# Performance work log

Measured on AMD Instinct MI355X. Metric: run time of the kernel, lower is better.

Reference implementation:

```python
import jax, jax.numpy as jnp
import numpy as np

WS = (8, 8)          # window_size -> S = 64
NUM_HEADS = 4
DIM = 128


def _relative_position_index(ws):
    wh, ww = ws
    coords = np.stack(np.meshgrid(np.arange(wh), np.arange(ww), indexing='ij'))  # (2,Wh,Ww)
    cf = coords.reshape(2, -1)                                   # (2, Wh*Ww)
    rel = cf[:, :, None] - cf[:, None, :]                        # (2, S, S)
    rel = rel.transpose(1, 2, 0).astype(np.int64)                # (S, S, 2)
    rel[:, :, 0] += wh - 1
    rel[:, :, 1] += ww - 1
    rel[:, :, 0] *= 2 * ww - 1
    return rel.sum(-1)                                           # (S, S)


def setup_inputs() -> dict:
    key = jax.random.key(0)
    k = jax.random.split(key, 6)
    B, S, N, C = 128, WS[0] * WS[1], 32, DIM
    num_rel = (2 * WS[0] - 1) * (2 * WS[1] - 1)
    return {
        'x': jax.random.normal(k[0], (B, S, N, C), dtype=jnp.float32),
        'qkv_w': jax.random.normal(k[1], (3 * C, C), dtype=jnp.float32) * 0.02,
        'qkv_b': jnp.zeros((3 * C,), dtype=jnp.float32),
        'proj_w': jax.random.normal(k[2], (C, C), dtype=jnp.float32) * 0.02,
        'proj_b': jnp.zeros((C,), dtype=jnp.float32),
        'bias_table': jax.random.normal(k[3], (num_rel, NUM_HEADS), dtype=jnp.float32) * 0.02,
    }


def reference(x, qkv_w, qkv_b, proj_w, proj_b, bias_table):
    B, S, N, C = x.shape
    H = NUM_HEADS
    D = N * C // H                      # effective head dim
    scale = (C // H) ** -0.5            # matches head_dim = dim // num_heads in __init__

    xf = x.reshape(B, S * N, C)
    qkv = xf @ qkv_w.T + qkv_b          # (B, S*N, 3C)
    qkv = qkv.reshape(B, S, 3, H, D).transpose(2, 0, 3, 1, 4)  # (3, B, H, S, D)
    q, k, v = qkv[0], qkv[1], qkv[2]

    rel_idx = jnp.asarray(_relative_position_index(WS))        # (S, S) int
    bias = bias_table[rel_idx.reshape(-1)].reshape(S, S, H).transpose(2, 0, 1)  # (H,S,S)

    attn = jnp.einsum('bhsd,bhtd->bhst', q, k) * scale + bias[None]
    attn = jax.nn.softmax(attn, axis=-1)

    out = jnp.einsum('bhst,bhtd->bhsd', attn, v)               # (B,H,S,D)
    out = out.transpose(0, 2, 1, 3).reshape(B, S * N, C)
    out = out @ proj_w.T + proj_b
    return out.reshape(B, S, N, C)
```

## Files before the change

### kernel.cpp

```cpp
#include <hip/hip_runtime.h>
#include <cmath>


typedef short bf16x8 __attribute__((ext_vector_type(8)));
typedef float f32x4  __attribute__((ext_vector_type(4)));
#define MFMA16 __builtin_amdgcn_mfma_f32_16x16x32_bf16

__device__ __forceinline__ unsigned rne16(float f) {
    unsigned u = __float_as_uint(f);
    return (u + 0x7fffu + ((u >> 16) & 1u)) & 0xffff0000u;
}
__device__ __forceinline__ void cvt8(float4 a, float4 b, bf16x8& H, bf16x8& L) {
    float f[8] = {a.x, a.y, a.z, a.w, b.x, b.y, b.z, b.w};
    #pragma unroll
    for (int i = 0; i < 8; ++i) {
        unsigned r = rne16(f[i]);
        H[i] = (short)(r >> 16);
        float fh = __uint_as_float(r);
        L[i] = (short)(rne16(f[i] - fh) >> 16);
    }
}
__device__ __forceinline__ void cvt8h(float4 a, float4 b, bf16x8& H) {
    float f[8] = {a.x, a.y, a.z, a.w, b.x, b.y, b.z, b.w};
    #pragma unroll
    for (int i = 0; i < 8; ++i) H[i] = (short)(rne16(f[i]) >> 16);
}

__global__ void split_w(const float* __restrict__ qw, unsigned short* __restrict__ wsp) {
    int idx = blockIdx.x * 256 + threadIdx.x;
    if (idx >= 49152) return;
    int j = idx >> 7, c = idx & 127;
    float v = qw[idx];
    unsigned r = rne16(v);
    unsigned rl = rne16(v - __uint_as_float(r));
    int dest = (((j >> 5) * 16 + (c >> 3)) * 32 + (j & 31)) * 8 + (c & 7);
    wsp[dest] = (unsigned short)(r >> 16);
    wsp[49152 + dest] = (unsigned short)(rl >> 16);
}
__global__ void split_pw(const float* __restrict__ pw, unsigned short* __restrict__ pwsp) {
    int idx = blockIdx.x * 256 + threadIdx.x;
    if (idx >= 16384) return;
    int cp = idx >> 7, c = idx & 127;
    float v = pw[idx];
    unsigned r = rne16(v);
    unsigned rl = rne16(v - __uint_as_float(r));
    int dest = ((c >> 3) * 128 + cp) * 8 + (c & 7);
    pwsp[dest] = (unsigned short)(r >> 16);
    pwsp[16384 + dest] = (unsigned short)(rl >> 16);
}

constexpr int A4_QC0 = 0,     A4_KC0 = 16640;
constexpr int A4_QC1 = 33280, A4_KC1 = 49920;
constexpr int A4_P   = 66560;
constexpr int A4_SMA = 74880;
constexpr int A4_SMB = 75392;
constexpr int A4_VC0 = 0,     A4_VC1 = 16640;
constexpr int A4_LDS = 75904;

__global__ __launch_bounds__(512, 4)
void attn_mfma4(const float* __restrict__ x,
                const float* __restrict__ qkv_b,
                const float* __restrict__ bias_table,
                const unsigned short* __restrict__ wsp,
                float* __restrict__ out)
{
    __shared__ __attribute__((aligned(128))) char lds[A4_LDS];
    const int tid = threadIdx.x;
    const int lane = tid & 63;
    const int w = tid >> 6;
    const int l15 = lane & 15, lg = lane >> 4;
    const int qt = w & 3, ch = w >> 2;
    const int rowbase = qt * 16;
    const int b = blockIdx.x >> 2, h = blockIdx.x & 3;
    const float* __restrict__ xb = x + (size_t)b * 262144;
    const float* xrow0 = xb + (size_t)(rowbase + l15) * 4096 + lg * 8;

    bf16x8 aH[4];
    bf16x8 kH[4];
    int cur_na = -1, cur_nk = -1;

    auto loadfrags = [&](int n0, bf16x8 (&H)[4]) {
        const float* p = xrow0 + (size_t)n0 * 128;
        #pragma unroll
        for (int ks = 0; ks < 4; ++ks) {
            float4 a = *(const float4*)(p + ks * 32);
            float4 c = *(const float4*)(p + ks * 32 + 4);
            cvt8h(a, c, H[ks]);
        }
    };

    auto prod64 = [&](const bf16x8 (&H)[4], int j0, f32x4 (&acc)[4]) {
        const unsigned short* wb = wsp + (size_t)(j0 >> 5) * 4096;
        #pragma unroll
        for (int ks = 0; ks < 4; ++ks) {
            #pragma unroll
            for (int ct = 0; ct < 4; ++ct) {
                int gct = ch * 4 + ct;
                int ro = (gct >> 1) * 4096 + ((ks * 4 + lg) * 32 + (gct & 1) * 16 + l15) * 8;
                bf16x8 bh = *(const bf16x8*)(wb + ro);
                acc[ct] = MFMA16(H[ks], bh, acc[ct], 0, 0, 0);
            }
        }
    };

    auto storeP64 = [&](int base, f32x4 (&acc)[4], int j0) {
        #pragma unroll
        for (int ct = 0; ct < 4; ++ct) {
            int d = (ch * 4 + ct) * 16 + l15;
            float bias = qkv_b[j0 + d];
            int dofs = (d >> 3) * 1040 + (d & 7) * 2;
            #pragma unroll
            for (int reg = 0; reg < 4; ++reg) {
                int s = rowbase + lg * 4 + reg;
                *(unsigned short*)(lds + base + dofs + s * 16) =
                    (unsigned short)(rne16(acc[ct][reg] + bias) >> 16);
            }
        }
    };

    f32x4 accQK[2];
    #pragma unroll
    for (int tt = 0; tt < 2; ++tt) accQK[tt] = (f32x4){0.f, 0.f, 0.f, 0.f};

    for (int cc = 0; cc < 8; ++cc) {
        int qcb = (cc & 1) ? A4_QC1 : A4_QC0;
        int kcb = (cc & 1) ? A4_KC1 : A4_KC0;
        int remq = h * 1024 + 128 * cc;
        int nq = remq / 384, j0q = remq - nq * 384;
        int remk = 4096 + h * 1024 + 128 * cc;
        int nk = remk / 384, j0k = remk - nk * 384;
        if (nq != cur_na) { loadfrags(nq, aH); cur_na = nq; }
        if (nk != cur_nk) { loadfrags(nk, kH); cur_nk = nk; }

        f32x4 qa[4];
        #pragma unroll
        for (int i = 0; i < 4; ++i) qa[i] = (f32x4){0.f, 0.f, 0.f, 0.f};
        prod64(aH, j0q, qa);
        storeP64(qcb, qa, j0q);

        f32x4 ka[4];
        #pragma unroll
        for (int i = 0; i < 4; ++i) ka[i] = (f32x4){0.f, 0.f, 0.f, 0.f};
        prod64(kH, j0k, ka);
        storeP64(kcb, ka, j0k);

        __syncthreads();

        #pragma unroll
        for (int kst = 0; kst < 4; ++kst) {
            int grp = (kst * 4 + lg) * 1040;
            bf16x8 qh = *(const bf16x8*)(lds + qcb + grp + (rowbase + l15) * 16);
            #pragma unroll
            for (int tt = 0; tt < 2; ++tt) {
                int trow = ((ch * 2 + tt) * 16 + l15) * 16;
                bf16x8 kh = *(const bf16x8*)(lds + kcb + grp + trow);
                accQK[tt] = MFMA16(qh, kh, accQK[tt], 0, 0, 0);
            }
        }
    }

    {
        const float scale = 0.17677669529663687f;
        float* smA = (float*)(lds + A4_SMA);
        float* smB = (float*)(lds + A4_SMB);
        float ex[4][2];
        #pragma unroll
        for (int reg = 0; reg < 4; ++reg) {
            int s = rowbase + lg * 4 + reg;
            int i1 = s >> 3, j1 = s & 7;
            float m = -1e30f;
            #pragma unroll
            for (int tt = 0; tt < 2; ++tt) {
                int t = (ch * 2 + tt) * 16 + l15;
                int i2 = t >> 3, j2 = t & 7;
                float L = accQK[tt][reg] * scale
                        + bias_table[((i1 - i2 + 7) * 15 + (j1 - j2 + 7)) * 4 + h];
                ex[reg][tt] = L;
                m = fmaxf(m, L);
            }
            m = fmaxf(m, __shfl_xor(m, 1));
            m = fmaxf(m, __shfl_xor(m, 2));
            m = fmaxf(m, __shfl_xor(m, 4));
            m = fmaxf(m, __shfl_xor(m, 8));
            if (l15 == 0) smA[ch * 64 + s] = m;
        }
        __syncthreads();
        #pragma unroll
        for (int reg = 0; reg < 4; ++reg) {
            int s = rowbase + lg * 4 + reg;
            float mg = fmaxf(smA[s], smA[64 + s]);
            float e0 = __expf(ex[reg][0] - mg);
            float e1 = __expf(ex[reg][1] - mg);
            ex[reg][0] = e0; ex[reg][1] = e1;
            float sum = e0 + e1;
            sum += __shfl_xor(sum, 1);
            sum += __shfl_xor(sum, 2);
            sum += __shfl_xor(sum, 4);
            sum += __shfl_xor(sum, 8);
            if (l15 == 0) smB[ch * 64 + s] = sum;
        }
        __syncthreads();
        #pragma unroll
        for (int reg = 0; reg < 4; ++reg) {
            int s = rowbase + lg * 4 + reg;
            float inv = 1.f / (smB[s] + smB[64 + s]);
            #pragma unroll
            for (int tt = 0; tt < 2; ++tt) {
                int t = (ch * 2 + tt) * 16 + l15;
                int off = (t >> 3) * 1040 + s * 16 + (t & 7) * 2;
                *(unsigned short*)(lds + A4_P + off) =
                    (unsigned short)(rne16(ex[reg][tt] * inv) >> 16);
            }
        }
    }

    cur_na = -1;
    float* ob = out + (size_t)b * 262144;
    for (int cc = 0; cc < 8; ++cc) {
        int vcb = (cc & 1) ? A4_VC1 : A4_VC0;
        int remv = 8192 + h * 1024 + 128 * cc;
        int nv = remv / 384, j0v = remv - nv * 384;
        if (nv != cur_na) { loadfrags(nv, aH); cur_na = nv; }

        f32x4 va[4];
        #pragma unroll
        for (int i = 0; i < 4; ++i) va[i] = (f32x4){0.f, 0.f, 0.f, 0.f};
        prod64(aH, j0v, va);

        #pragma unroll
        for (int ct = 0; ct < 4; ++ct) {
            int d = (ch * 4 + ct) * 16 + l15;
            float bias = qkv_b[j0v + d];
            #pragma unroll
            for (int reg = 0; reg < 4; ++reg) {
                int t = rowbase + lg * 4 + reg;
                int off = (t >> 3) * 2080 + d * 16 + (t & 7) * 2;
                *(unsigned short*)(lds + vcb + off) =
                    (unsigned short)(rne16(va[ct][reg] + bias) >> 16);
            }
        }
        __syncthreads();

        f32x4 o[4];
        #pragma unroll
        for (int i = 0; i < 4; ++i) o[i] = (f32x4){0.f, 0.f, 0.f, 0.f};
        #pragma unroll
        for (int kst = 0; kst < 2; ++kst) {
            bf16x8 pf = *(const bf16x8*)(lds + A4_P + (kst * 4 + lg) * 1040 + (rowbase + l15) * 16);
            int vgrp = (kst * 4 + lg) * 2080;
            #pragma unroll
            for (int dt = 0; dt < 4; ++dt) {
                int drow = ((ch * 4 + dt) * 16 + l15) * 16;
                bf16x8 vh = *(const bf16x8*)(lds + vcb + vgrp + drow);
                o[dt] = MFMA16(pf, vh, o[dt], 0, 0, 0);
            }
        }

        #pragma unroll
        for (int reg = 0; reg < 4; ++reg) {
            int s = rowbase + lg * 4 + reg;
            float* orow = ob + (size_t)(s * 32 + h * 8 + cc) * 128;
            #pragma unroll
            for (int dt = 0; dt < 4; ++dt)
                orow[(ch * 4 + dt) * 16 + l15] = o[dt][reg];
        }
    }
}

__global__ __launch_bounds__(256, 4)
void proj_mfma(const unsigned short* __restrict__ pwsp,
               const float* __restrict__ pb,
               float* __restrict__ io)
{
    const int tid = threadIdx.x;
    const int lane = tid & 63;
    const int w = tid >> 6;
    const int l15 = lane & 15, lg = lane >> 4;
    const size_t rbase = (size_t)blockIdx.x * 64 + w * 16;

    const float* rp = io + (rbase + l15) * 128 + lg * 8;
    bf16x8 aH[4], aL[4];
    #pragma unroll
    for (int ks = 0; ks < 4; ++ks) {
        float4 a = *(const float4*)(rp + ks * 32);
        float4 c = *(const float4*)(rp + ks * 32 + 4);
        cvt8(a, c, aH[ks], aL[ks]);
    }

    f32x4 acc[8];
    #pragma unroll
    for (int i = 0; i < 8; ++i) acc[i] = (f32x4){0.f, 0.f, 0.f, 0.f};

    #pragma unroll
    for (int ks = 0; ks < 4; ++ks) {
        #pragma unroll
        for (int ct = 0; ct < 8; ++ct) {
            int ro = ((ks * 4 + lg) * 128 + ct * 16 + l15) * 8;
            bf16x8 bh = *(const bf16x8*)(pwsp + ro);
            bf16x8 bl = *(const bf16x8*)(pwsp + 16384 + ro);
            acc[ct] = MFMA16(aH[ks], bh, acc[ct], 0, 0, 0);
            acc[ct] = MFMA16(aH[ks], bl, acc[ct], 0, 0, 0);
            acc[ct] = MFMA16(aL[ks], bh, acc[ct], 0, 0, 0);
        }
    }

    #pragma unroll
    for (int ct = 0; ct < 8; ++ct) {
        float bias = pb[ct * 16 + l15];
        #pragma unroll
        for (int reg = 0; reg < 4; ++reg)
            io[(rbase + lg * 4 + reg) * 128 + ct * 16 + l15] = acc[ct][reg] + bias;
    }
}

constexpr int QC_OFF = 0;
constexpr int KC_OFF = 8320;
constexpr int VC_OFF = 24960;
constexpr int P_OFF  = 41856;
constexpr int LDS_TOT = 50176;

__global__ __launch_bounds__(256, 2)
void attn_mfma(const float* __restrict__ x,
               const float* __restrict__ qkv_b,
               const float* __restrict__ bias_table,
               const unsigned short* __restrict__ wsp,
               float* __restrict__ out)
{
    __shared__ __attribute__((aligned(128))) char lds[LDS_TOT];
    const int tid = threadIdx.x;
    const int lane = tid & 63;
    const int w = tid >> 6;
    const int l15 = lane & 15, lg = lane >> 4;
    const int rowbase = 16 * w;
    const int b = blockIdx.x >> 2, h = blockIdx.x & 3;
    const float* __restrict__ xb = x + (size_t)b * 262144;
    const float* xrow0 = xb + ((size_t)(rowbase + l15) * 32) * 128 + lg * 8;

    bf16x8 aH[4], aL[4];
    bf16x8 kH[4], kL[4];
    int cur_na = -1, cur_nk = -1;

    auto loadfrags = [&](int n0, bf16x8 (&H)[4], bf16x8 (&L)[4]) {
        const float* p = xrow0 + (size_t)n0 * 128;
        #pragma unroll
        for (int ks = 0; ks < 4; ++ks) {
            float4 a = *(const float4*)(p + ks * 32);
            float4 c = *(const float4*)(p + ks * 32 + 4);
            cvt8(a, c, H[ks], L[ks]);
        }
    };

    auto mm_band = [&](const bf16x8 (&H)[4], const bf16x8 (&L)[4], int band,
                       f32x4& a0, f32x4& a1) {
        const unsigned short* wb = wsp + (size_t)band * 4096;
        #pragma unroll
        for (int ks = 0; ks < 4; ++ks) {
            int ro = ((ks * 4 + lg) * 32 + l15) * 8;
            bf16x8 b0h = *(const bf16x8*)(wb + ro);
            bf16x8 b0l = *(const bf16x8*)(wb + 49152 + ro);
            bf16x8 b1h = *(const bf16x8*)(wb + ro + 128);
            bf16x8 b1l = *(const bf16x8*)(wb + 49152 + ro + 128);
            a0 = MFMA16(H[ks], b0h, a0, 0, 0, 0);
            a0 = MFMA16(H[ks], b0l, a0, 0, 0, 0);
            a0 = MFMA16(L[ks], b0h, a0, 0, 0, 0);
            a1 = MFMA16(H[ks], b1h, a1, 0, 0, 0);
            a1 = MFMA16(H[ks], b1l, a1, 0, 0, 0);
            a1 = MFMA16(L[ks], b1h, a1, 0, 0, 0);
        }
    };

    auto store_rc = [&](char* base, f32x4 a0, f32x4 a1, float b0, float b1) {
        #pragma unroll
        for (int reg = 0; reg < 4; ++reg) {
            int s = rowbase + lg * 4 + reg;
            {
                float v = a0[reg] + b0;
                int i = l15;
                int off = (i >> 3) * 1040 + s * 16 + (i & 7) * 2;
                unsigned r = rne16(v);
                *(unsigned short*)(base + off) = (unsigned short)(r >> 16);
                *(unsigned short*)(base + 4160 + off) =
                    (unsigned short)(rne16(v - __uint_as_float(r)) >> 16);
            }
            {
                float v = a1[reg] + b1;
                int i = 16 + l15;
                int off = (i >> 3) * 1040 + s * 16 + (i & 7) * 2;
                unsigned r = rne16(v);
                *(unsigned short*)(base + off) = (unsigned short)(r >> 16);
                *(unsigned short*)(base + 4160 + off) =
                    (unsigned short)(rne16(v - __uint_as_float(r)) >> 16);
            }
        }
    };

    f32x4 accQK[4];
    #pragma unroll
    for (int tt = 0; tt < 4; ++tt) accQK[tt] = (f32x4){0.f, 0.f, 0.f, 0.f};

    int buf = 0;
    for (int ccc = 0; ccc < 32; ++ccc) {
        int remq = h * 1024 + 32 * ccc;
        int nq = remq / 384, j0q = remq - nq * 384, bandq = j0q >> 5;
        int remk = 4096 + h * 1024 + 32 * ccc;
        int nk = remk / 384, j0k = remk - nk * 384, bandk = j0k >> 5;
        if (nq != cur_na) { loadfrags(nq, aH, aL); cur_na = nq; }
        if (nk != cur_nk) { loadfrags(nk, kH, kL); cur_nk = nk; }

        f32x4 q0 = (f32x4){0.f,0.f,0.f,0.f}, q1 = (f32x4){0.f,0.f,0.f,0.f};
        mm_band(aH, aL, bandq, q0, q1);
        store_rc(lds + QC_OFF, q0, q1, qkv_b[j0q + l15], qkv_b[j0q + 16 + l15]);

        f32x4 k0 = (f32x4){0.f,0.f,0.f,0.f}, k1 = (f32x4){0.f,0.f,0.f,0.f};
        mm_band(kH, kL, bandk, k0, k1);
        store_rc(lds + KC_OFF + buf * 8320, k0, k1, qkv_b[j0k + l15], qkv_b[j0k + 16 + l15]);

        __syncthreads();

        const char* qc = lds + QC_OFF + lg * 1040 + (rowbase + l15) * 16;
        bf16x8 qah = *(const bf16x8*)qc;
        bf16x8 qal = *(const bf16x8*)(qc + 4160);
        #pragma unroll
        for (int tt = 0; tt < 4; ++tt) {
            const char* kc = lds + KC_OFF + buf * 8320 + lg * 1040 + (tt * 16 + l15) * 16;
            bf16x8 kbh = *(const bf16x8*)kc;
            bf16x8 kbl = *(const bf16x8*)(kc + 4160);
            accQK[tt] = MFMA16(qah, kbh, accQK[tt], 0, 0, 0);
            accQK[tt] = MFMA16(qah, kbl, accQK[tt], 0, 0, 0);
            accQK[tt] = MFMA16(qal, kbh, accQK[tt], 0, 0, 0);
        }
        buf ^= 1;
    }

    {
        const float scale = 0.17677669529663687f;
        #pragma unroll
        for (int reg = 0; reg < 4; ++reg) {
            int s = rowbase + lg * 4 + reg;
            int i1 = s >> 3, j1 = s & 7;
            float Lv[4];
            float m = -1e30f;
            #pragma unroll
            for (int tt = 0; tt < 4; ++tt) {
                int t = tt * 16 + l15;
                int i2 = t >> 3, j2 = t & 7;
                float L = accQK[tt][reg] * scale
                        + bias_table[((i1 - i2 + 7) * 15 + (j1 - j2 + 7)) * 4 + h];
                Lv[tt] = L;
                m = fmaxf(m, L);
            }
            m = fmaxf(m, __shfl_xor(m, 1));
            m = fmaxf(m, __shfl_xor(m, 2));
            m = fmaxf(m, __shfl_xor(m, 4));
            m = fmaxf(m, __shfl_xor(m, 8));
            float sum = 0.f;
            #pragma unroll
            for (int tt = 0; tt < 4; ++tt) { Lv[tt] = __expf(Lv[tt] - m); sum += Lv[tt]; }
            sum += __shfl_xor(sum, 1);
            sum += __shfl_xor(sum, 2);
            sum += __shfl_xor(sum, 4);
            sum += __shfl_xor(sum, 8);
            float inv = 1.f / sum;
            #pragma unroll
            for (int tt = 0; tt < 4; ++tt) {
                int t = tt * 16 + l15;
                int off = (t >> 3) * 1040 + s * 16 + (t & 7) * 2;
                *(unsigned short*)(lds + P_OFF + off) = (unsigned short)(rne16(Lv[tt] * inv) >> 16);
            }
        }
    }

    cur_na = -1;
    int bufv = 0;
    float* ob = out + (size_t)b * 262144;
    for (int ccc = 0; ccc < 32; ++ccc) {
        int remv = 8192 + h * 1024 + 32 * ccc;
        int nv = remv / 384, j0v = remv - nv * 384, bandv = j0v >> 5;
        if (nv != cur_na) { loadfrags(nv, aH, aL); cur_na = nv; }

        f32x4 v0 = (f32x4){0.f,0.f,0.f,0.f}, v1 = (f32x4){0.f,0.f,0.f,0.f};
        mm_band(aH, aL, bandv, v0, v1);
        {
            char* base = lds + VC_OFF + bufv * 8448;
            float b0 = qkv_b[j0v + l15], b1 = qkv_b[j0v + 16 + l15];
            #pragma unroll
            for (int reg = 0; reg < 4; ++reg) {
                int t = rowbase + lg * 4 + reg;
                {
                    float v = v0[reg] + b0;
                    int i = l15;
                    int off = (t >> 3) * 528 + i * 16 + (t & 7) * 2;
                    unsigned r = rne16(v);
                    *(unsigned short*)(base + off) = (unsigned short)(r >> 16);
                    *(unsigned short*)(base + 4224 + off) =
                        (unsigned short)(rne16(v - __uint_as_float(r)) >> 16);
                }
                {
                    float v = v1[reg] + b1;
                    int i = 16 + l15;
                    int off = (t >> 3) * 528 + i * 16 + (t & 7) * 2;
                    unsigned r = rne16(v);
                    *(unsigned short*)(base + off) = (unsigned short)(r >> 16);
                    *(unsigned short*)(base + 4224 + off) =
                        (unsigned short)(rne16(v - __uint_as_float(r)) >> 16);
                }
            }
        }
        __syncthreads();

        f32x4 o0 = (f32x4){0.f,0.f,0.f,0.f}, o1 = (f32x4){0.f,0.f,0.f,0.f};
        #pragma unroll
        for (int ks = 0; ks < 2; ++ks) {
            bf16x8 pf = *(const bf16x8*)(lds + P_OFF + (ks * 4 + lg) * 1040 + (rowbase + l15) * 16);
            const char* vb = lds + VC_OFF + bufv * 8448 + (ks * 4 + lg) * 528;
            bf16x8 v0h = *(const bf16x8*)(vb + l15 * 16);
            bf16x8 v0l = *(const bf16x8*)(vb + 4224 + l15 * 16);
            bf16x8 v1h = *(const bf16x8*)(vb + (16 + l15) * 16);
            bf16x8 v1l = *(const bf16x8*)(vb + 4224 + (16 + l15) * 16);
            o0 = MFMA16(pf, v0h, o0, 0, 0, 0);
            o0 = MFMA16(pf, v0l, o0, 0, 0, 0);
            o1 = MFMA16(pf, v1h, o1, 0, 0, 0);
            o1 = MFMA16(pf, v1l, o1, 0, 0, 0);
        }
        bufv ^= 1;

        #pragma unroll
        for (int reg = 0; reg < 4; ++reg) {
            int s = rowbase + lg * 4 + reg;
            {
                int d = 32 * ccc + l15;
                ob[(s * 32 + h * 8 + (d >> 7)) * 128 + (d & 127)] = o0[reg];
            }
            {
                int d = 32 * ccc + 16 + l15;
                ob[(s * 32 + h * 8 + (d >> 7)) * 128 + (d & 127)] = o1[reg];
            }
        }
    }
}

constexpr int LDS_B = 128 * 132 + 64 * 132;

__global__ __launch_bounds__(256, 1)
void proj_inplace(const float* __restrict__ pw,
                  const float* __restrict__ pb,
                  float* __restrict__ io)
{
    __shared__ float lds[LDS_B];
    float* pwt  = lds;
    float* rows = lds + 128 * 132;
    const int tid = threadIdx.x;

    for (int idx = tid; idx < 128 * 128; idx += 256) {
        const int c = idx >> 7, cp = idx & 127;
        pwt[cp * 132 + c] = pw[idx];
    }
    const int rb = tid >> 5;
    const int cg = tid & 31;
    const float4 pbv = *(const float4*)(pb + cg * 4);

    for (int it = 0; it < 8; ++it) {
        const size_t base = ((size_t)blockIdx.x * 8 + it) * 64;
        __syncthreads();
        for (int f = tid; f < 64 * 32; f += 256) {
            const int r = f >> 5, c4 = f & 31;
            *(float4*)(rows + r * 132 + c4 * 4) =
                *(const float4*)(io + (base + r) * 128 + c4 * 4);
        }
        __syncthreads();
        float acc[8][4] = {};
        #pragma unroll 2
        for (int cp = 0; cp < 128; ++cp) {
            const float4 wv = *(const float4*)(pwt + cp * 132 + cg * 4);
            #pragma unroll
            for (int rr = 0; rr < 8; ++rr) {
                const float xv = rows[(rb * 8 + rr) * 132 + cp];
                acc[rr][0] += xv * wv.x;
                acc[rr][1] += xv * wv.y;
                acc[rr][2] += xv * wv.z;
                acc[rr][3] += xv * wv.w;
            }
        }
        #pragma unroll
        for (int rr = 0; rr < 8; ++rr) {
            float4 o;
            o.x = acc[rr][0] + pbv.x;
            o.y = acc[rr][1] + pbv.y;
            o.z = acc[rr][2] + pbv.z;
            o.w = acc[rr][3] + pbv.w;
            *(float4*)(io + (base + rb * 8 + rr) * 128 + cg * 4) = o;
        }
    }
}

extern "C" void kernel_launch(void* const* d_in, const int* in_sizes, int n_in,
                              void* d_out, int out_size, void* d_ws, size_t ws_size,
                              hipStream_t stream)
{
    const float* x          = (const float*)d_in[0];
    const float* qkv_w      = (const float*)d_in[1];
    const float* qkv_b      = (const float*)d_in[2];
    const float* proj_w     = (const float*)d_in[3];
    const float* proj_b     = (const float*)d_in[4];
    const float* bias_table = (const float*)d_in[5];
    float* out = (float*)d_out;

    if (ws_size >= 262144 && d_ws != nullptr) {
        unsigned short* wsp = (unsigned short*)d_ws;
        split_w<<<dim3(192), dim3(256), 0, stream>>>(qkv_w, wsp);
        split_pw<<<dim3(64), dim3(256), 0, stream>>>(proj_w, wsp + 98304);
        attn_mfma4<<<dim3(512), dim3(512), 0, stream>>>(x, qkv_b, bias_table, wsp, out);
        proj_mfma<<<dim3(4096), dim3(256), 0, stream>>>(wsp + 98304, proj_b, out);
    } else if (ws_size >= 196608 && d_ws != nullptr) {
        unsigned short* wsp = (unsigned short*)d_ws;
        split_w<<<dim3(192), dim3(256), 0, stream>>>(qkv_w, wsp);
        attn_mfma<<<dim3(512), dim3(256), 0, stream>>>(x, qkv_b, bias_table, wsp, out);
        proj_inplace<<<dim3(512), dim3(256), 0, stream>>>(proj_w, proj_b, out);
    }
}
```

Baseline: 202.0 us.

## Software-pipeline Q/K and V projection chunks with double-buffered LDS

Restructures both chunk loops in the attention kernel so that the projection for chunk cc+1 is computed and written to the alternate LDS buffer while the MFMA consumption of chunk cc proceeds. Each iteration still ends with one barrier. The aim is to overlap global loads and projection math with the QK^T and PV MFMAs, which removes the serialisation between the produce and consume phases of each chunk. The cost is higher register pressure, since both the producer's accumulators and the consumer's fragments are live at the same time.

Measured after the change: 192.5 us. 4.7% less time.

```diff
diff --git a/kernel.cpp b/kernel.cpp
--- a/kernel.cpp
+++ b/kernel.cpp
@@ -49,22 +49,22 @@
     pwsp[16384 + dest] = (unsigned short)(rl >> 16);
 }
 
-constexpr int A4_QC0 = 0,     A4_KC0 = 16640;
-constexpr int A4_QC1 = 33280, A4_KC1 = 49920;
-constexpr int A4_P   = 66560;
-constexpr int A4_SMA = 74880;
-constexpr int A4_SMB = 75392;
-constexpr int A4_VC0 = 0,     A4_VC1 = 16640;
-constexpr int A4_LDS = 75904;
+constexpr int A5_QC0 = 0,     A5_KC0 = 16640;
+constexpr int A5_QC1 = 33280, A5_KC1 = 49920;
+constexpr int A5_P   = 66560;
+constexpr int A5_SMA = 74880;
+constexpr int A5_SMB = 75392;
+constexpr int A5_VC0 = 0,     A5_VC1 = 16640;
+constexpr int A5_LDS = 75904;
 
 __global__ __launch_bounds__(512, 4)
-void attn_mfma4(const float* __restrict__ x,
+void attn_mfma5(const float* __restrict__ x,
                 const float* __restrict__ qkv_b,
                 const float* __restrict__ bias_table,
                 const unsigned short* __restrict__ wsp,
                 float* __restrict__ out)
 {
-    __shared__ __attribute__((aligned(128))) char lds[A4_LDS];
+    __shared__ __attribute__((aligned(128))) char lds[A5_LDS];
     const int tid = threadIdx.x;
     const int lane = tid & 63;
     const int w = tid >> 6;
@@ -118,34 +118,37 @@
         }
     };
 
-    f32x4 accQK[2];
-    #pragma unroll
-    for (int tt = 0; tt < 2; ++tt) accQK[tt] = (f32x4){0.f, 0.f, 0.f, 0.f};
-
-    for (int cc = 0; cc < 8; ++cc) {
-        int qcb = (cc & 1) ? A4_QC1 : A4_QC0;
-        int kcb = (cc & 1) ? A4_KC1 : A4_KC0;
+    auto prodQK = [&](int cc) {
         int remq = h * 1024 + 128 * cc;
         int nq = remq / 384, j0q = remq - nq * 384;
         int remk = 4096 + h * 1024 + 128 * cc;
         int nk = remk / 384, j0k = remk - nk * 384;
         if (nq != cur_na) { loadfrags(nq, aH); cur_na = nq; }
         if (nk != cur_nk) { loadfrags(nk, kH); cur_nk = nk; }
-
         f32x4 qa[4];
         #pragma unroll
         for (int i = 0; i < 4; ++i) qa[i] = (f32x4){0.f, 0.f, 0.f, 0.f};
         prod64(aH, j0q, qa);
-        storeP64(qcb, qa, j0q);
-
+        storeP64((cc & 1) ? A5_QC1 : A5_QC0, qa, j0q);
         f32x4 ka[4];
         #pragma unroll
         for (int i = 0; i < 4; ++i) ka[i] = (f32x4){0.f, 0.f, 0.f, 0.f};
         prod64(kH, j0k, ka);
-        storeP64(kcb, ka, j0k);
-
-        __syncthreads();
-
+        storeP64((cc & 1) ? A5_KC1 : A5_KC0, ka, j0k);
+    };
+
+    f32x4 accQK[2];
+    #pragma unroll
+    for (int tt = 0; tt < 2; ++tt) accQK[tt] = (f32x4){0.f, 0.f, 0.f, 0.f};
+
+    prodQK(0);
+    __syncthreads();
+
+    for (int cc = 0; cc < 8; ++cc) {
+        if (cc < 7) prodQK(cc + 1);
+
+        int qcb = (cc & 1) ? A5_QC1 : A5_QC0;
+        int kcb = (cc & 1) ? A5_KC1 : A5_KC0;
         #pragma unroll
         for (int kst = 0; kst < 4; ++kst) {
             int grp = (kst * 4 + lg) * 1040;
@@ -157,12 +160,13 @@
                 accQK[tt] = MFMA16(qh, kh, accQK[tt], 0, 0, 0);
             }
         }
+        __syncthreads();
     }
 
     {
         const float scale = 0.17677669529663687f;
-        float* smA = (float*)(lds + A4_SMA);
-        float* smB = (float*)(lds + A4_SMB);
+        float* smA = (float*)(lds + A5_SMA);
+        float* smB = (float*)(lds + A5_SMB);
         float ex[4][2];
         #pragma unroll
         for (int reg = 0; reg < 4; ++reg) {
@@ -208,7 +212,7 @@
             for (int tt = 0; tt < 2; ++tt) {
                 int t = (ch * 2 + tt) * 16 + l15;
                 int off = (t >> 3) * 1040 + s * 16 + (t & 7) * 2;
-                *(unsigned short*)(lds + A4_P + off) =
+                *(unsigned short*)(lds + A5_P + off) =
                     (unsigned short)(rne16(ex[reg][tt] * inv) >> 16);
             }
         }
@@ -216,17 +220,16 @@
 
     cur_na = -1;
     float* ob = out + (size_t)b * 262144;
-    for (int cc = 0; cc < 8; ++cc) {
-        int vcb = (cc & 1) ? A4_VC1 : A4_VC0;
+
+    auto prodV = [&](int cc) {
         int remv = 8192 + h * 1024 + 128 * cc;
         int nv = remv / 384, j0v = remv - nv * 384;
         if (nv != cur_na) { loadfrags(nv, aH); cur_na = nv; }
-
         f32x4 va[4];
         #pragma unroll
         for (int i = 0; i < 4; ++i) va[i] = (f32x4){0.f, 0.f, 0.f, 0.f};
         prod64(aH, j0v, va);
-
+        int vcb = (cc & 1) ? A5_VC1 : A5_VC0;
         #pragma unroll
         for (int ct = 0; ct < 4; ++ct) {
             int d = (ch * 4 + ct) * 16 + l15;
@@ -239,14 +242,21 @@
                     (unsigned short)(rne16(va[ct][reg] + bias) >> 16);
             }
         }
-        __syncthreads();
-
+    };
+
+    prodV(0);
+    __syncthreads();
+
+    for (int cc = 0; cc < 8; ++cc) {
+        if (cc < 7) prodV(cc + 1);
+
+        int vcb = (cc & 1) ? A5_VC1 : A5_VC0;
         f32x4 o[4];
         #pragma unroll
         for (int i = 0; i < 4; ++i) o[i] = (f32x4){0.f, 0.f, 0.f, 0.f};
         #pragma unroll
         for (int kst = 0; kst < 2; ++kst) {
-            bf16x8 pf = *(const bf16x8*)(lds + A4_P + (kst * 4 + lg) * 1040 + (rowbase + l15) * 16);
+            bf16x8 pf = *(const bf16x8*)(lds + A5_P + (kst * 4 + lg) * 1040 + (rowbase + l15) * 16);
             int vgrp = (kst * 4 + lg) * 2080;
             #pragma unroll
             for (int dt = 0; dt < 4; ++dt) {
@@ -264,6 +274,7 @@
             for (int dt = 0; dt < 4; ++dt)
                 orow[(ch * 4 + dt) * 16 + l15] = o[dt][reg];
         }
+        __syncthreads();
     }
 }
 
@@ -609,7 +620,7 @@
         unsigned short* wsp = (unsigned short*)d_ws;
         split_w<<<dim3(192), dim3(256), 0, stream>>>(qkv_w, wsp);
         split_pw<<<dim3(64), dim3(256), 0, stream>>>(proj_w, wsp + 98304);
-        attn_mfma4<<<dim3(512), dim3(512), 0, stream>>>(x, qkv_b, bias_table, wsp, out);
+        attn_mfma5<<<dim3(512), dim3(512), 0, stream>>>(x, qkv_b, bias_table, wsp, out);
         proj_mfma<<<dim3(4096), dim3(256), 0, stream>>>(wsp + 98304, proj_b, out);
     } else if (ws_size >= 196608 && d_ws != nullptr) {
         unsigned short* wsp = (unsigned short*)d_ws;
```

## Single-buffer LDS and drop fragment caching in attention kernel to raise occupancy

Applied to the files above, without the earlier changes.

Replaces the double-buffered Q/K/V LDS chunks with single buffers and adds an extra barrier per iteration, roughly halving shared memory per block. The cached bf16 fragment arrays for the x rows are removed, so x is reloaded and converted on every chunk, which cuts register pressure. Launch bounds are raised to target more resident blocks. The cost is more barriers, lost overlap between chunks, and redundant global loads and conversions. With only 512 blocks in the grid, higher occupancy may give little benefit.

New measurement: 275.3 us. 36.2% more time.

```diff
diff --git a/kernel.cpp b/kernel.cpp
--- a/kernel.cpp
+++ b/kernel.cpp
@@ -49,22 +49,22 @@
     pwsp[16384 + dest] = (unsigned short)(rl >> 16);
 }
 
-constexpr int A4_QC0 = 0,     A4_KC0 = 16640;
-constexpr int A4_QC1 = 33280, A4_KC1 = 49920;
-constexpr int A4_P   = 66560;
-constexpr int A4_SMA = 74880;
-constexpr int A4_SMB = 75392;
-constexpr int A4_VC0 = 0,     A4_VC1 = 16640;
-constexpr int A4_LDS = 75904;
-
-__global__ __launch_bounds__(512, 4)
-void attn_mfma4(const float* __restrict__ x,
+constexpr int A8_QC  = 0;
+constexpr int A8_KC  = 16640;
+constexpr int A8_P   = 33280;
+constexpr int A8_SMA = 41600;
+constexpr int A8_SMB = 42112;
+constexpr int A8_VC  = 0;
+constexpr int A8_LDS = 42624;
+
+__global__ __launch_bounds__(512, 6)
+void attn_mfma8(const float* __restrict__ x,
                 const float* __restrict__ qkv_b,
                 const float* __restrict__ bias_table,
                 const unsigned short* __restrict__ wsp,
                 float* __restrict__ out)
 {
-    __shared__ __attribute__((aligned(128))) char lds[A4_LDS];
+    __shared__ __attribute__((aligned(128))) char lds[A8_LDS];
     const int tid = threadIdx.x;
     const int lane = tid & 63;
     const int w = tid >> 6;
@@ -75,21 +75,19 @@
     const float* __restrict__ xb = x + (size_t)b * 262144;
     const float* xrow0 = xb + (size_t)(rowbase + l15) * 4096 + lg * 8;
 
-    bf16x8 aH[4];
-    bf16x8 kH[4];
-    int cur_na = -1, cur_nk = -1;
-
-    auto loadfrags = [&](int n0, bf16x8 (&H)[4]) {
+    bf16x8 F[4];
+
+    auto loadfrags = [&](int n0) {
         const float* p = xrow0 + (size_t)n0 * 128;
         #pragma unroll
         for (int ks = 0; ks < 4; ++ks) {
             float4 a = *(const float4*)(p + ks * 32);
             float4 c = *(const float4*)(p + ks * 32 + 4);
-            cvt8h(a, c, H[ks]);
+            cvt8h(a, c, F[ks]);
         }
     };
 
-    auto prod64 = [&](const bf16x8 (&H)[4], int j0, f32x4 (&acc)[4]) {
+    auto prod64 = [&](int j0, f32x4 (&acc)[4]) {
         const unsigned short* wb = wsp + (size_t)(j0 >> 5) * 4096;
         #pragma unroll
         for (int ks = 0; ks < 4; ++ks) {
@@ -98,7 +96,7 @@
                 int gct = ch * 4 + ct;
                 int ro = (gct >> 1) * 4096 + ((ks * 4 + lg) * 32 + (gct & 1) * 16 + l15) * 8;
                 bf16x8 bh = *(const bf16x8*)(wb + ro);
-                acc[ct] = MFMA16(H[ks], bh, acc[ct], 0, 0, 0);
+                acc[ct] = MFMA16(F[ks], bh, acc[ct], 0, 0, 0);
             }
         }
     };
@@ -123,46 +121,45 @@
     for (int tt = 0; tt < 2; ++tt) accQK[tt] = (f32x4){0.f, 0.f, 0.f, 0.f};
 
     for (int cc = 0; cc < 8; ++cc) {
-        int qcb = (cc & 1) ? A4_QC1 : A4_QC0;
-        int kcb = (cc & 1) ? A4_KC1 : A4_KC0;
         int remq = h * 1024 + 128 * cc;
         int nq = remq / 384, j0q = remq - nq * 384;
         int remk = 4096 + h * 1024 + 128 * cc;
         int nk = remk / 384, j0k = remk - nk * 384;
-        if (nq != cur_na) { loadfrags(nq, aH); cur_na = nq; }
-        if (nk != cur_nk) { loadfrags(nk, kH); cur_nk = nk; }
-
+
+        loadfrags(nq);
         f32x4 qa[4];
         #pragma unroll
         for (int i = 0; i < 4; ++i) qa[i] = (f32x4){0.f, 0.f, 0.f, 0.f};
-        prod64(aH, j0q, qa);
-        storeP64(qcb, qa, j0q);
-
+        prod64(j0q, qa);
+        storeP64(A8_QC, qa, j0q);
+
+        loadfrags(nk);
         f32x4 ka[4];
         #pragma unroll
         for (int i = 0; i < 4; ++i) ka[i] = (f32x4){0.f, 0.f, 0.f, 0.f};
-        prod64(kH, j0k, ka);
-        storeP64(kcb, ka, j0k);
+        prod64(j0k, ka);
+        storeP64(A8_KC, ka, j0k);
 
         __syncthreads();
 
         #pragma unroll
         for (int kst = 0; kst < 4; ++kst) {
             int grp = (kst * 4 + lg) * 1040;
-            bf16x8 qh = *(const bf16x8*)(lds + qcb + grp + (rowbase + l15) * 16);
+            bf16x8 qh = *(const bf16x8*)(lds + A8_QC + grp + (rowbase + l15) * 16);
             #pragma unroll
             for (int tt = 0; tt < 2; ++tt) {
                 int trow = ((ch * 2 + tt) * 16 + l15) * 16;
-                bf16x8 kh = *(const bf16x8*)(lds + kcb + grp + trow);
+                bf16x8 kh = *(const bf16x8*)(lds + A8_KC + grp + trow);
                 accQK[tt] = MFMA16(qh, kh, accQK[tt], 0, 0, 0);
             }
         }
+        __syncthreads();
     }
 
     {
         const float scale = 0.17677669529663687f;
-        float* smA = (float*)(lds + A4_SMA);
-        float* smB = (float*)(lds + A4_SMB);
+        float* smA = (float*)(lds + A8_SMA);
+        float* smB = (float*)(lds + A8_SMB);
         float ex[4][2];
         #pragma unroll
         for (int reg = 0; reg < 4; ++reg) {
@@ -208,24 +205,22 @@
             for (int tt = 0; tt < 2; ++tt) {
                 int t = (ch * 2 + tt) * 16 + l15;
                 int off = (t >> 3) * 1040 + s * 16 + (t & 7) * 2;
-                *(unsigned short*)(lds + A4_P + off) =
+                *(unsigned short*)(lds + A8_P + off) =
                     (unsigned short)(rne16(ex[reg][tt] * inv) >> 16);
             }
         }
     }
 
-    cur_na = -1;
     float* ob = out + (size_t)b * 262144;
     for (int cc = 0; cc < 8; ++cc) {
-        int vcb = (cc & 1) ? A4_VC1 : A4_VC0;
         int remv = 8192 + h * 1024 + 128 * cc;
         int nv = remv / 384, j0v = remv - nv * 384;
-        if (nv != cur_na) { loadfrags(nv, aH); cur_na = nv; }
-
+
+        loadfrags(nv);
         f32x4 va[4];
         #pragma unroll
         for (int i = 0; i < 4; ++i) va[i] = (f32x4){0.f, 0.f, 0.f, 0.f};
-        prod64(aH, j0v, va);
+        prod64(j0v, va);
 
         #pragma unroll
         for (int ct = 0; ct < 4; ++ct) {
@@ -235,7 +230,7 @@
             for (int reg = 0; reg < 4; ++reg) {
                 int t = rowbase + lg * 4 + reg;
                 int off = (t >> 3) * 2080 + d * 16 + (t & 7) * 2;
-                *(unsigned short*)(lds + vcb + off) =
+                *(unsigned short*)(lds + A8_VC + off) =
                     (unsigned short)(rne16(va[ct][reg] + bias) >> 16);
             }
         }
@@ -246,12 +241,12 @@
         for (int i = 0; i < 4; ++i) o[i] = (f32x4){0.f, 0.f, 0.f, 0.f};
         #pragma unroll
         for (int kst = 0; kst < 2; ++kst) {
-            bf16x8 pf = *(const bf16x8*)(lds + A4_P + (kst * 4 + lg) * 1040 + (rowbase + l15) * 16);
+            bf16x8 pf = *(const bf16x8*)(lds + A8_P + (kst * 4 + lg) * 1040 + (rowbase + l15) * 16);
             int vgrp = (kst * 4 + lg) * 2080;
             #pragma unroll
             for (int dt = 0; dt < 4; ++dt) {
                 int drow = ((ch * 4 + dt) * 16 + l15) * 16;
-                bf16x8 vh = *(const bf16x8*)(lds + vcb + vgrp + drow);
+                bf16x8 vh = *(const bf16x8*)(lds + A8_VC + vgrp + drow);
                 o[dt] = MFMA16(pf, vh, o[dt], 0, 0, 0);
             }
         }
@@ -264,6 +259,7 @@
             for (int dt = 0; dt < 4; ++dt)
                 orow[(ch * 4 + dt) * 16 + l15] = o[dt][reg];
         }
+        __syncthreads();
     }
 }
 
@@ -607,10 +603,11 @@
 
     if (ws_size >= 262144 && d_ws != nullptr) {
         unsigned short* wsp = (unsigned short*)d_ws;
+        unsigned short* pwsp = wsp + 98304;
         split_w<<<dim3(192), dim3(256), 0, stream>>>(qkv_w, wsp);
-        split_pw<<<dim3(64), dim3(256), 0, stream>>>(proj_w, wsp + 98304);
-        attn_mfma4<<<dim3(512), dim3(512), 0, stream>>>(x, qkv_b, bias_table, wsp, out);
-        proj_mfma<<<dim3(4096), dim3(256), 0, stream>>>(wsp + 98304, proj_b, out);
+        split_pw<<<dim3(64), dim3(256), 0, stream>>>(proj_w, pwsp);
+        attn_mfma8<<<dim3(512), dim3(512), 0, stream>>>(x, qkv_b, bias_table, wsp, out);
+        proj_mfma<<<dim3(4096), dim3(256), 0, stream>>>(pwsp, proj_b, out);
     } else if (ws_size >= 196608 && d_ws != nullptr) {
         unsigned short* wsp = (unsigned short*)d_ws;
         split_w<<<dim3(192), dim3(256), 0, stream>>>(qkv_w, wsp);
```
